# Kernel optimization log

Hardware: AMD Instinct MI355X
Metric: run time of the kernel (lower is better)

Reference implementation:

```python
import jax, jax.numpy as jnp
import numpy as np

N = 12  # mmse_block_size
REAL_SIZE = N * (N + 1) // 2  # 78: diag + strict lower
IMAG_SIZE = N * (N - 1) // 2  # 66: strict lower only
ROWS, COLS = jnp.tril_indices(N)        # row-major (i, j<=i) matches torch loop order
ROWS_S, COLS_S = jnp.tril_indices(N, -1)  # strict lower, row-major, matches imag loop
DIAG_MASK = jnp.eye(N, dtype=bool)


def _mlp(x, W1, b1, W2, b2, W3, b3):
    h = jax.nn.relu(x @ W1 + b1)
    h = jax.nn.relu(h @ W2 + b2)
    return h @ W3 + b3


def _cholesky_outer(flat):
    # flat: [B, REAL_SIZE + IMAG_SIZE] -> [B, N, N] complex, L @ L^H
    B = flat.shape[0]
    L_real = jnp.zeros((B, N, N), flat.dtype).at[:, ROWS, COLS].set(flat[:, :REAL_SIZE])
    L_real = jnp.where(DIAG_MASK, jax.nn.softplus(L_real), L_real)
    L_imag = jnp.zeros((B, N, N), flat.dtype).at[:, ROWS_S, COLS_S].set(
        flat[:, REAL_SIZE:REAL_SIZE + IMAG_SIZE])
    L = L_real + 1j * L_imag
    return jnp.einsum('bij,bkj->bik', L, jnp.conj(L))


def setup_inputs() -> dict:
    key = jax.random.key(0)
    ks = jax.random.split(key, 13)
    L, H, OUT = 4096, 64, REAL_SIZE + IMAG_SIZE
    sc = lambda k, shp, fan: (jax.random.normal(k, shp, jnp.float32) / np.sqrt(fan))
    return {
        'channel_stats': jax.random.normal(ks[0], (8192, L), jnp.float32),
        'WC1': sc(ks[1], (L, H), L), 'bC1': jnp.zeros((H,), jnp.float32),
        'WC2': sc(ks[2], (H, H), H), 'bC2': jnp.zeros((H,), jnp.float32),
        'WC3': sc(ks[3], (H, OUT), H), 'bC3': jnp.zeros((OUT,), jnp.float32),
        'WR1': sc(ks[4], (L, H), L), 'bR1': jnp.zeros((H,), jnp.float32),
        'WR2': sc(ks[5], (H, H), H), 'bR2': jnp.zeros((H,), jnp.float32),
        'WR3': sc(ks[6], (H, OUT), H), 'bR3': jnp.zeros((OUT,), jnp.float32),
    }


def reference(channel_stats, WC1, bC1, WC2, bC2, WC3, bC3,
              WR1, bR1, WR2, bR2, WR3, bR3):
    C_flat = _mlp(channel_stats, WC1, bC1, WC2, bC2, WC3, bC3)
    R_flat = _mlp(channel_stats, WR1, bR1, WR2, bR2, WR3, bR3)
    C = _cholesky_outer(C_flat)
    R = _cholesky_outer(R_flat)
    return C, R
```

## Files before the change

kernel.cpp:

```cpp
#include <hip/hip_runtime.h>
#include <stdint.h>

#define M_ROWS 8192
#define K_DIM  4096
#define NCOLS  128
#define OUTD   144
#define PLANE  1179648

typedef __attribute__((ext_vector_type(4))) float  float4v;
typedef __attribute__((ext_vector_type(8))) short  short8v;
typedef __attribute__((ext_vector_type(4))) short  short4v;

static __device__ __forceinline__ unsigned short f2bf(float f) {
    unsigned int u = __builtin_bit_cast(unsigned int, f);
    u += 0x7FFFu + ((u >> 16) & 1u);
    return (unsigned short)(u >> 16);
}

__global__ __launch_bounds__(256) void wt_kernel(
    const float* __restrict__ WC1, const float* __restrict__ WR1,
    unsigned short* __restrict__ Wt) {
    __shared__ float tile[64][65];
    const float* src = (blockIdx.y == 0) ? WC1 : WR1;
    const int k0 = blockIdx.x * 64;
    const int t = threadIdx.x;
    const int j = t & 63, q = t >> 6;
#pragma unroll
    for (int p = 0; p < 16; ++p) {
        int i = p * 4 + q;
        tile[i][j] = src[(size_t)(k0 + i) * 64 + j];
    }
    __syncthreads();
#pragma unroll
    for (int p = 0; p < 16; ++p) {
        int n = p * 4 + q;
        Wt[(size_t)(blockIdx.y * 64 + n) * K_DIM + k0 + j] = f2bf(tile[j][n]);
    }
}

__global__ __launch_bounds__(256) void fused_kernel(
    const float* __restrict__ X, const unsigned short* __restrict__ Wt,
    const float* __restrict__ bC1, const float* __restrict__ bR1,
    const float* __restrict__ WC2, const float* __restrict__ bC2,
    const float* __restrict__ WR2, const float* __restrict__ bR2,
    const float* __restrict__ WC3, const float* __restrict__ bC3,
    const float* __restrict__ WR3, const float* __restrict__ bR3,
    unsigned short* __restrict__ OUT) {
    __shared__ __align__(16) char smem[41216];
    unsigned short* Asm_ = (unsigned short*)smem;
    unsigned short* Bsm_ = Asm_ + 16 * 72;
    float* hs  = (float*)smem;
    float* W2s = hs + 16 * 132;
    float* fl  = W2s;

    const int tid  = threadIdx.x;
    const int lane = tid & 63;
    const int w    = tid >> 6;
    const int r0   = blockIdx.x * 16;
    const int m    = lane & 15, q = lane >> 4;
    const int ar   = tid >> 4, akc = tid & 15;

    float4v acc0 = {0.f, 0.f, 0.f, 0.f};
    float4v acc1 = {0.f, 0.f, 0.f, 0.f};

    for (int kk = 0; kk < K_DIM; kk += 64) {
        float4 x = *(const float4*)(X + (size_t)(r0 + ar) * K_DIM + kk + akc * 4);
        short4v s;
        s.x = (short)f2bf(x.x); s.y = (short)f2bf(x.y);
        s.z = (short)f2bf(x.z); s.w = (short)f2bf(x.w);
        uint4 breg[4];
#pragma unroll
        for (int p = 0; p < 4; ++p) {
            int ci = p * 256 + tid;
            int n = ci >> 3, k8 = ci & 7;
            breg[p] = *(const uint4*)(Wt + (size_t)n * K_DIM + kk + k8 * 8);
        }
        *(short4v*)&Asm_[ar * 72 + akc * 4] = s;
#pragma unroll
        for (int p = 0; p < 4; ++p) {
            int ci = p * 256 + tid;
            int n = ci >> 3, k8 = ci & 7;
            *(uint4*)&Bsm_[n * 72 + k8 * 8] = breg[p];
        }
        __syncthreads();
#pragma unroll
        for (int ks = 0; ks < 2; ++ks) {
            short8v a  = *(const short8v*)&Asm_[m * 72 + ks * 32 + q * 8];
            short8v b0 = *(const short8v*)&Bsm_[(w * 32 + m) * 72 + ks * 32 + q * 8];
            short8v b1 = *(const short8v*)&Bsm_[(w * 32 + 16 + m) * 72 + ks * 32 + q * 8];
            acc0 = __builtin_amdgcn_mfma_f32_16x16x32_bf16(a, b0, acc0, 0, 0, 0);
            acc1 = __builtin_amdgcn_mfma_f32_16x16x32_bf16(a, b1, acc1, 0, 0, 0);
        }
        __syncthreads();
    }
    {
        const int c0 = w * 32 + m;
        const int c1 = w * 32 + 16 + m;
        const float bv0 = (c0 < 64) ? bC1[c0] : bR1[c0 - 64];
        const float bv1 = (c1 < 64) ? bC1[c1] : bR1[c1 - 64];
#pragma unroll
        for (int i = 0; i < 4; ++i) {
            int r = q * 4 + i;
            float v0 = acc0[i] + bv0; v0 = v0 > 0.f ? v0 : 0.f;
            float v1 = acc1[i] + bv1; v1 = v1 > 0.f ? v1 : 0.f;
            hs[r * 132 + c0] = v0;
            hs[r * 132 + c1] = v1;
        }
    }
#pragma unroll
    for (int p = 0; p < 8; ++p) {
        int fi = p * 256 + tid;
        int k = fi >> 5, c4 = fi & 31;
        int c = c4 * 4;
        const float* wsrc = (c < 64) ? (WC2 + (size_t)k * 64 + c)
                                     : (WR2 + (size_t)k * 64 + (c - 64));
        *(float4*)&W2s[k * 128 + c] = *(const float4*)wsrc;
    }
    __syncthreads();

    const int rg = tid >> 5;
    const int cg = tid & 31;
    const int koff2 = (cg < 16) ? 0 : 64;
    float acc2[2][4];
    {
        int c = cg * 4;
        const float* bsrc = (c < 64) ? (bC2 + c) : (bR2 + (c - 64));
#pragma unroll
        for (int i = 0; i < 2; ++i)
#pragma unroll
            for (int j = 0; j < 4; ++j) acc2[i][j] = bsrc[j];
    }
    for (int k = 0; k < 64; ++k) {
        float4 wv = *(const float4*)&W2s[k * 128 + cg * 4];
#pragma unroll
        for (int i = 0; i < 2; ++i) {
            float a = hs[(rg * 2 + i) * 132 + koff2 + k];
            acc2[i][0] += a * wv.x; acc2[i][1] += a * wv.y;
            acc2[i][2] += a * wv.z; acc2[i][3] += a * wv.w;
        }
    }
    float h2r[2][4];
#pragma unroll
    for (int i = 0; i < 2; ++i)
#pragma unroll
        for (int j = 0; j < 4; ++j)
            h2r[i][j] = acc2[i][j] > 0.f ? acc2[i][j] : 0.f;
    __syncthreads();
#pragma unroll
    for (int i = 0; i < 2; ++i) {
        float4 v; v.x = h2r[i][0]; v.y = h2r[i][1]; v.z = h2r[i][2]; v.w = h2r[i][3];
        *(float4*)&hs[(rg * 2 + i) * 132 + cg * 4] = v;
    }
    __syncthreads();

    for (int pass = 0; pass < 3; ++pass) {
        int c = pass * 128 + cg * 4;
        if (c < 288) {
            const int brn = (c >= 144);
            const int cl = c - (brn ? 144 : 0);
            const float* W3 = brn ? WR3 : WC3;
            const float* b3 = brn ? bR3 : bC3;
            const int ko = brn ? 64 : 0;
            float a3[2][4];
#pragma unroll
            for (int i = 0; i < 2; ++i)
#pragma unroll
                for (int j = 0; j < 4; ++j) a3[i][j] = b3[cl + j];
            for (int k = 0; k < 64; ++k) {
                float4 wv = *(const float4*)(W3 + (size_t)k * OUTD + cl);
#pragma unroll
                for (int i = 0; i < 2; ++i) {
                    float a = hs[(rg * 2 + i) * 132 + ko + k];
                    a3[i][0] += a * wv.x; a3[i][1] += a * wv.y;
                    a3[i][2] += a * wv.z; a3[i][3] += a * wv.w;
                }
            }
#pragma unroll
            for (int i = 0; i < 2; ++i) {
                float4 v; v.x = a3[i][0]; v.y = a3[i][1]; v.z = a3[i][2]; v.w = a3[i][3];
                *(float4*)&fl[(rg * 2 + i) * 288 + c] = v;
            }
        }
    }
    __syncthreads();

#pragma unroll
    for (int p = 0; p < 2; ++p) {
        int idx = p * 256 + tid;
        if (idx < 384) {
            int r = idx / 24, rem = idx % 24;
            int brn = rem / 12, ii = rem % 12;
            float* f = &fl[r * 288 + brn * 144];
            int d = ii * (ii + 1) / 2 + ii;
            float xv = f[d];
            f[d] = (xv > 20.f) ? xv : log1pf(expf(xv));
        }
    }
    __syncthreads();

    for (int task = tid; task < 16 * 2 * 78; task += 256) {
        int r = task / 156, rem = task % 156;
        int brn = rem / 78, p = rem % 78;
        int i = 0;
        while (p >= (i + 1) * (i + 2) / 2) ++i;
        int j = p - i * (i + 1) / 2;
        const float* f = &fl[r * 288 + brn * 144];
        const float* g = f + 78;
        const int ti = i * (i + 1) / 2, tj = j * (j + 1) / 2;
        const int si = i * (i - 1) / 2, sj = j * (j - 1) / 2;
        float re = 0.f, im = 0.f;
        for (int k = 0; k <= j; ++k) {
            float ar_ = f[ti + k];
            float ai  = (k == i) ? 0.f : g[si + k];
            float br_ = f[tj + k];
            float bi  = (k == j) ? 0.f : g[sj + k];
            re += ar_ * br_ + ai * bi;
            im += ai * br_ - ar_ * bi;
        }
        unsigned short reb = f2bf(re);
        unsigned short imb = f2bf(im);
        unsigned short imn = f2bf(-im);
        size_t base = brn ? (size_t)(2 * PLANE) : 0;
        size_t q1 = (size_t)(r0 + r) * 144 + (size_t)(i * 12 + j);
        OUT[base + 2 * q1]     = imb;
        OUT[base + 2 * q1 + 1] = reb;
        if (i != j) {
            size_t q2 = (size_t)(r0 + r) * 144 + (size_t)(j * 12 + i);
            OUT[base + 2 * q2]     = imn;
            OUT[base + 2 * q2 + 1] = reb;
        }
    }
}

extern "C" void kernel_launch(void* const* d_in, const int* in_sizes, int n_in,
                              void* d_out, int out_size, void* d_ws, size_t ws_size,
                              hipStream_t stream) {
    const float* X   = (const float*)d_in[0];
    const float* WC1 = (const float*)d_in[1];
    const float* bC1 = (const float*)d_in[2];
    const float* WC2 = (const float*)d_in[3];
    const float* bC2 = (const float*)d_in[4];
    const float* WC3 = (const float*)d_in[5];
    const float* bC3 = (const float*)d_in[6];
    const float* WR1 = (const float*)d_in[7];
    const float* bR1 = (const float*)d_in[8];
    const float* WR2 = (const float*)d_in[9];
    const float* bR2 = (const float*)d_in[10];
    const float* WR3 = (const float*)d_in[11];
    const float* bR3 = (const float*)d_in[12];

    unsigned short* Wt = (unsigned short*)d_ws;
    unsigned short* OUT = (unsigned short*)d_out;

    wt_kernel<<<dim3(64, 2), 256, 0, stream>>>(WC1, WR1, Wt);
    fused_kernel<<<M_ROWS / 16, 256, 0, stream>>>(
        X, Wt, bC1, bR1, WC2, bC2, WR2, bR2, WC3, bC3, WR3, bR3, OUT);
}
```

Baseline: 282.6 us.

## Double-buffer K loop via registers, 512 threads, wider K tiles, packed output stores

The fused kernel now uses 512 threads per block with 128-wide K tiles. Global loads for the next tile are issued into a second register set before the current tile's MFMAs run, so memory latency overlaps with compute. Each wave now owns a single 16-column MFMA tile, the per-thread epilogue work is halved, and the bf16 real/imag output pairs are written as single 32-bit stores. In exchange, per-thread register pressure rises and the 4-waves-per-SIMD launch bound may force spilling.

Result: slower. 430.3 us (+52.3%).

```diff
diff --git a/kernel.cpp b/kernel.cpp
--- a/kernel.cpp
+++ b/kernel.cpp
@@ -38,7 +38,7 @@
     }
 }
 
-__global__ __launch_bounds__(256) void fused_kernel(
+__global__ __launch_bounds__(512, 4) void fused_kernel(
     const float* __restrict__ X, const unsigned short* __restrict__ Wt,
     const float* __restrict__ bC1, const float* __restrict__ bR1,
     const float* __restrict__ WC2, const float* __restrict__ bC2,
@@ -48,7 +48,7 @@
     unsigned short* __restrict__ OUT) {
     __shared__ __align__(16) char smem[41216];
     unsigned short* Asm_ = (unsigned short*)smem;
-    unsigned short* Bsm_ = Asm_ + 16 * 72;
+    unsigned short* Bsm_ = Asm_ + 16 * 136;
     float* hs  = (float*)smem;
     float* W2s = hs + 16 * 132;
     float* fl  = W2s;
@@ -58,58 +58,69 @@
     const int w    = tid >> 6;
     const int r0   = blockIdx.x * 16;
     const int m    = lane & 15, q = lane >> 4;
-    const int ar   = tid >> 4, akc = tid & 15;
-
-    float4v acc0 = {0.f, 0.f, 0.f, 0.f};
-    float4v acc1 = {0.f, 0.f, 0.f, 0.f};
-
-    for (int kk = 0; kk < K_DIM; kk += 64) {
-        float4 x = *(const float4*)(X + (size_t)(r0 + ar) * K_DIM + kk + akc * 4);
+    const int ar   = tid >> 5, akc = tid & 31;
+
+    float4v acc = {0.f, 0.f, 0.f, 0.f};
+
+    const float* xp = X + (size_t)(r0 + ar) * K_DIM + akc * 4;
+    const unsigned short* wp = Wt + (size_t)(tid >> 4) * K_DIM + (tid & 15) * 8;
+    unsigned short* aw = &Asm_[ar * 136 + akc * 4];
+    unsigned short* bw = &Bsm_[(tid >> 4) * 136 + (tid & 15) * 8];
+
+    float4 xa, xb; uint4 ba[4], bb[4];
+
+    auto LOADT = [&](int kk, float4& x, uint4* b) {
+        x = *(const float4*)(xp + kk);
+#pragma unroll
+        for (int p = 0; p < 4; ++p)
+            b[p] = *(const uint4*)(wp + (size_t)p * 32 * K_DIM + kk);
+    };
+    auto STORET = [&](const float4& x, const uint4* b) {
         short4v s;
         s.x = (short)f2bf(x.x); s.y = (short)f2bf(x.y);
         s.z = (short)f2bf(x.z); s.w = (short)f2bf(x.w);
-        uint4 breg[4];
-#pragma unroll
-        for (int p = 0; p < 4; ++p) {
-            int ci = p * 256 + tid;
-            int n = ci >> 3, k8 = ci & 7;
-            breg[p] = *(const uint4*)(Wt + (size_t)n * K_DIM + kk + k8 * 8);
-        }
-        *(short4v*)&Asm_[ar * 72 + akc * 4] = s;
-#pragma unroll
-        for (int p = 0; p < 4; ++p) {
-            int ci = p * 256 + tid;
-            int n = ci >> 3, k8 = ci & 7;
-            *(uint4*)&Bsm_[n * 72 + k8 * 8] = breg[p];
-        }
-        __syncthreads();
-#pragma unroll
-        for (int ks = 0; ks < 2; ++ks) {
-            short8v a  = *(const short8v*)&Asm_[m * 72 + ks * 32 + q * 8];
-            short8v b0 = *(const short8v*)&Bsm_[(w * 32 + m) * 72 + ks * 32 + q * 8];
-            short8v b1 = *(const short8v*)&Bsm_[(w * 32 + 16 + m) * 72 + ks * 32 + q * 8];
-            acc0 = __builtin_amdgcn_mfma_f32_16x16x32_bf16(a, b0, acc0, 0, 0, 0);
-            acc1 = __builtin_amdgcn_mfma_f32_16x16x32_bf16(a, b1, acc1, 0, 0, 0);
-        }
-        __syncthreads();
-    }
+        *(short4v*)aw = s;
+#pragma unroll
+        for (int p = 0; p < 4; ++p)
+            *(uint4*)(bw + p * 32 * 136) = b[p];
+    };
+    auto MF = [&]() {
+#pragma unroll
+        for (int ks = 0; ks < 4; ++ks) {
+            short8v a = *(const short8v*)&Asm_[m * 136 + ks * 32 + q * 8];
+            short8v b = *(const short8v*)&Bsm_[(w * 16 + m) * 136 + ks * 32 + q * 8];
+            acc = __builtin_amdgcn_mfma_f32_16x16x32_bf16(a, b, acc, 0, 0, 0);
+        }
+    };
+
+    LOADT(0, xa, ba);
+#pragma unroll 1
+    for (int kk = 0; kk < K_DIM; kk += 256) {
+        STORET(xa, ba);
+        __syncthreads();
+        LOADT(kk + 128, xb, bb);
+        MF();
+        __syncthreads();
+        STORET(xb, bb);
+        __syncthreads();
+        if (kk + 256 < K_DIM) LOADT(kk + 256, xa, ba);
+        MF();
+        __syncthreads();
+    }
+
     {
-        const int c0 = w * 32 + m;
-        const int c1 = w * 32 + 16 + m;
-        const float bv0 = (c0 < 64) ? bC1[c0] : bR1[c0 - 64];
-        const float bv1 = (c1 < 64) ? bC1[c1] : bR1[c1 - 64];
+        const int c = w * 16 + m;
+        const float bv = (c < 64) ? bC1[c] : bR1[c - 64];
 #pragma unroll
         for (int i = 0; i < 4; ++i) {
             int r = q * 4 + i;
-            float v0 = acc0[i] + bv0; v0 = v0 > 0.f ? v0 : 0.f;
-            float v1 = acc1[i] + bv1; v1 = v1 > 0.f ? v1 : 0.f;
-            hs[r * 132 + c0] = v0;
-            hs[r * 132 + c1] = v1;
-        }
-    }
-#pragma unroll
-    for (int p = 0; p < 8; ++p) {
-        int fi = p * 256 + tid;
+            float v = acc[i] + bv; v = v > 0.f ? v : 0.f;
+            hs[r * 132 + c] = v;
+        }
+    }
+#pragma unroll
+    for (int p = 0; p < 4; ++p) {
+        int fi = p * 512 + tid;
         int k = fi >> 5, c4 = fi & 31;
         int c = c4 * 4;
         const float* wsrc = (c < 64) ? (WC2 + (size_t)k * 64 + c)
@@ -121,38 +132,29 @@
     const int rg = tid >> 5;
     const int cg = tid & 31;
     const int koff2 = (cg < 16) ? 0 : 64;
-    float acc2[2][4];
+    float acc2[4];
     {
         int c = cg * 4;
         const float* bsrc = (c < 64) ? (bC2 + c) : (bR2 + (c - 64));
 #pragma unroll
-        for (int i = 0; i < 2; ++i)
-#pragma unroll
-            for (int j = 0; j < 4; ++j) acc2[i][j] = bsrc[j];
+        for (int j = 0; j < 4; ++j) acc2[j] = bsrc[j];
     }
     for (int k = 0; k < 64; ++k) {
         float4 wv = *(const float4*)&W2s[k * 128 + cg * 4];
-#pragma unroll
-        for (int i = 0; i < 2; ++i) {
-            float a = hs[(rg * 2 + i) * 132 + koff2 + k];
-            acc2[i][0] += a * wv.x; acc2[i][1] += a * wv.y;
-            acc2[i][2] += a * wv.z; acc2[i][3] += a * wv.w;
-        }
-    }
-    float h2r[2][4];
-#pragma unroll
-    for (int i = 0; i < 2; ++i)
-#pragma unroll
-        for (int j = 0; j < 4; ++j)
-            h2r[i][j] = acc2[i][j] > 0.f ? acc2[i][j] : 0.f;
-    __syncthreads();
-#pragma unroll
-    for (int i = 0; i < 2; ++i) {
-        float4 v; v.x = h2r[i][0]; v.y = h2r[i][1]; v.z = h2r[i][2]; v.w = h2r[i][3];
-        *(float4*)&hs[(rg * 2 + i) * 132 + cg * 4] = v;
-    }
-    __syncthreads();
-
+        float a = hs[rg * 132 + koff2 + k];
+        acc2[0] += a * wv.x; acc2[1] += a * wv.y;
+        acc2[2] += a * wv.z; acc2[3] += a * wv.w;
+    }
+    float4 h2v;
+    h2v.x = acc2[0] > 0.f ? acc2[0] : 0.f;
+    h2v.y = acc2[1] > 0.f ? acc2[1] : 0.f;
+    h2v.z = acc2[2] > 0.f ? acc2[2] : 0.f;
+    h2v.w = acc2[3] > 0.f ? acc2[3] : 0.f;
+    __syncthreads();
+    *(float4*)&hs[rg * 132 + cg * 4] = h2v;
+    __syncthreads();
+
+#pragma unroll 1
     for (int pass = 0; pass < 3; ++pass) {
         int c = pass * 128 + cg * 4;
         if (c < 288) {
@@ -161,44 +163,33 @@
             const float* W3 = brn ? WR3 : WC3;
             const float* b3 = brn ? bR3 : bC3;
             const int ko = brn ? 64 : 0;
-            float a3[2][4];
-#pragma unroll
-            for (int i = 0; i < 2; ++i)
-#pragma unroll
-                for (int j = 0; j < 4; ++j) a3[i][j] = b3[cl + j];
+            float a3[4];
+#pragma unroll
+            for (int j = 0; j < 4; ++j) a3[j] = b3[cl + j];
             for (int k = 0; k < 64; ++k) {
                 float4 wv = *(const float4*)(W3 + (size_t)k * OUTD + cl);
-#pragma unroll
-                for (int i = 0; i < 2; ++i) {
-                    float a = hs[(rg * 2 + i) * 132 + ko + k];
-                    a3[i][0] += a * wv.x; a3[i][1] += a * wv.y;
-                    a3[i][2] += a * wv.z; a3[i][3] += a * wv.w;
-                }
+                float a = hs[rg * 132 + ko + k];
+                a3[0] += a * wv.x; a3[1] += a * wv.y;
+                a3[2] += a * wv.z; a3[3] += a * wv.w;
             }
-#pragma unroll
-            for (int i = 0; i < 2; ++i) {
-                float4 v; v.x = a3[i][0]; v.y = a3[i][1]; v.z = a3[i][2]; v.w = a3[i][3];
-                *(float4*)&fl[(rg * 2 + i) * 288 + c] = v;
-            }
-        }
-    }
-    __syncthreads();
-
-#pragma unroll
-    for (int p = 0; p < 2; ++p) {
-        int idx = p * 256 + tid;
-        if (idx < 384) {
-            int r = idx / 24, rem = idx % 24;
-            int brn = rem / 12, ii = rem % 12;
-            float* f = &fl[r * 288 + brn * 144];
-            int d = ii * (ii + 1) / 2 + ii;
-            float xv = f[d];
-            f[d] = (xv > 20.f) ? xv : log1pf(expf(xv));
-        }
-    }
-    __syncthreads();
-
-    for (int task = tid; task < 16 * 2 * 78; task += 256) {
+            float4 v; v.x = a3[0]; v.y = a3[1]; v.z = a3[2]; v.w = a3[3];
+            *(float4*)&fl[rg * 288 + c] = v;
+        }
+    }
+    __syncthreads();
+
+    if (tid < 384) {
+        int r = tid / 24, rem = tid % 24;
+        int brn = rem / 12, ii = rem % 12;
+        float* f = &fl[r * 288 + brn * 144];
+        int d = ii * (ii + 1) / 2 + ii;
+        float xv = f[d];
+        f[d] = (xv > 20.f) ? xv : log1pf(expf(xv));
+    }
+    __syncthreads();
+
+    unsigned int* O32 = (unsigned int*)OUT;
+    for (int task = tid; task < 16 * 2 * 78; task += 512) {
         int r = task / 156, rem = task % 156;
         int brn = rem / 78, p = rem % 78;
         int i = 0;
@@ -217,17 +208,15 @@
             re += ar_ * br_ + ai * bi;
             im += ai * br_ - ar_ * bi;
         }
-        unsigned short reb = f2bf(re);
-        unsigned short imb = f2bf(im);
-        unsigned short imn = f2bf(-im);
-        size_t base = brn ? (size_t)(2 * PLANE) : 0;
+        unsigned int reb = (unsigned int)f2bf(re);
+        unsigned int imb = (unsigned int)f2bf(im);
+        unsigned int imn = (unsigned int)f2bf(-im);
+        size_t base = brn ? (size_t)PLANE : 0;
         size_t q1 = (size_t)(r0 + r) * 144 + (size_t)(i * 12 + j);
-        OUT[base + 2 * q1]     = imb;
-        OUT[base + 2 * q1 + 1] = reb;
+        O32[base + q1] = imb | (reb << 16);
         if (i != j) {
             size_t q2 = (size_t)(r0 + r) * 144 + (size_t)(j * 12 + i);
-            OUT[base + 2 * q2]     = imn;
-            OUT[base + 2 * q2 + 1] = reb;
+            O32[base + q2] = imn | (reb << 16);
         }
     }
 }
@@ -253,6 +242,6 @@
     unsigned short* OUT = (unsigned short*)d_out;
 
     wt_kernel<<<dim3(64, 2), 256, 0, stream>>>(WC1, WR1, Wt);
-    fused_kernel<<<M_ROWS / 16, 256, 0, stream>>>(
+    fused_kernel<<<M_ROWS / 16, 512, 0, stream>>>(
         X, Wt, bC1, bR1, WC2, bC2, WR2, bR2, WC3, bC3, WR3, bR3, OUT);
 }
```
